# Kernel tuning notes

Hardware: AMD Instinct MI355X
Metric: run time of the kernel (lower is better)

## Reference

```python
import jax, jax.numpy as jnp
import numpy as np

D = 32      # bond_dim
N = 784     # 28*28 physical sites
HALF = 392  # single_rank = rank // 2
L = 10      # labels
B = 128     # batch


def setup_inputs() -> dict:
    key = jax.random.key(0)
    k0, k1, k2, k3, k4, k5 = jax.random.split(key, 6)
    # per-site 2-component input features; components sum to 1 so the
    # 392-step transfer-matrix product stays numerically stable in fp32
    u = jax.random.uniform(k0, (B, N), dtype=jnp.float32)
    x = jnp.stack([u, 1.0 - u], axis=-1)  # (B, 784, 2)

    eye = jnp.eye(D, dtype=jnp.float32)[None, :, None, :]  # (1, D, 1, D)
    a0 = jax.random.normal(k1, (D, 2), dtype=jnp.float32) / np.float32(np.sqrt(D))
    cores_left = eye + 0.01 * jax.random.normal(k2, (HALF - 1, D, 2, D), dtype=jnp.float32)
    core_mid = 0.05 * jax.random.normal(k3, (D, L, D), dtype=jnp.float32)
    cores_right = eye + 0.01 * jax.random.normal(k4, (HALF - 1, D, 2, D), dtype=jnp.float32)
    a_end = jax.random.normal(k5, (D, 2), dtype=jnp.float32) / np.float32(np.sqrt(D))
    return {"x": x, "a0": a0, "cores_left": cores_left, "core_mid": core_mid,
            "cores_right": cores_right, "a_end": a_end}


def reference(x, a0, cores_left, core_mid, cores_right, a_end):
    # ---- left half: nodes 0..391 contracted with inputs 0..391 ----
    v0 = jnp.einsum('dp,bp->bd', a0, x[:, 0])                       # (B, D)
    # input-contracted transfer matrices for nodes 1..391
    Ml = jnp.einsum('nlpr,bnp->nblr', cores_left, x[:, 1:HALF])      # (391, B, D, D)

    def step_left(c, M):
        return jnp.einsum('bl,blr->br', c, M), None

    left, _ = jax.lax.scan(step_left, v0, Ml)                        # (B, D)

    # ---- right half: nodes 393..784 contracted with inputs 392..783 ----
    r0 = jnp.einsum('dp,bp->bd', a_end, x[:, N - 1])                 # (B, D)
    Mr = jnp.einsum('nlpr,bnp->nblr', cores_right, x[:, HALF:N - 1])  # (391, B, D, D)

    def step_right(c, M):
        return jnp.einsum('blr,br->bl', M, c), None

    right, _ = jax.lax.scan(step_right, r0, Mr, reverse=True)        # (B, D)

    # ---- middle label node: original does einsum('a,aba,a->b') (diagonal!) ----
    mid_diag = jnp.einsum('aba->ab', core_mid)                       # (D, L)
    return jnp.einsum('ba,ba,ac->bc', left, right, mid_diag)         # (B, 10)
```

## Files before the change

kernel.cpp:

```cpp
#include <hip/hip_runtime.h>

#define NSTEP 391
#define NB 128
#define NGRP 16

typedef __attribute__((ext_vector_type(8))) short s8v;
typedef __attribute__((ext_vector_type(16))) float f32x16;

typedef const __attribute__((address_space(1))) void* gas_ptr;
typedef __attribute__((address_space(3))) void* las_ptr;

union I4S8 { int4 i; s8v v; };
union W4S8 { int w[4]; s8v v; };

#define WAITVM(N) do { asm volatile("s_waitcnt vmcnt(" #N ")" ::: "memory"); \
                       __builtin_amdgcn_sched_barrier(0); } while (0)
#define LGKM0     do { asm volatile("s_waitcnt lgkmcnt(0)" ::: "memory");   \
                       __builtin_amdgcn_sched_barrier(0); } while (0)
#define SBAR      do { __builtin_amdgcn_s_barrier();                        \
                       __builtin_amdgcn_sched_barrier(0); } while (0)

__device__ __forceinline__ int pack_hi(float a, float b) {
    return (__float_as_int(b) & 0xffff0000) | ((unsigned)__float_as_int(a) >> 16);
}
__device__ __forceinline__ float trunc_bf(float a) {
    return __int_as_float(__float_as_int(a) & 0xffff0000);
}
__device__ __forceinline__ int cvtpk(float a, float b) {
    int r;
    asm("v_cvt_pk_bf16_f32 %0, %1, %2" : "=v"(r) : "v"(a), "v"(b));
    return r;
}

__global__ __launch_bounds__(256) void prep(
    const float* __restrict__ coresL, const float* __restrict__ coresR,
    int* __restrict__ aprep) {
    const int bid = blockIdx.x;
    const int side = bid >= NSTEP;
    const int t = bid - side * NSTEP;
    const float* st = (side ? coresR : coresL) + t * 2048;
    int* out = aprep + (size_t)(side * NSTEP + t) * 2048;
    for (int o = threadIdx.x; o < 2048; o += 256) {
        const int f = o >> 8, lane = (o >> 2) & 63, w = o & 3;
        const int part = f >> 2, p = (f >> 1) & 1, j = f & 1;
        const int h = lane >> 5, c = lane & 31;
        const int k0 = j * 16 + h * 8 + w * 2;
        float e0, e1;
        if (!side) { e0 = st[c * 64 + p * 32 + k0];  e1 = st[c * 64 + p * 32 + k0 + 1]; }
        else       { e0 = st[k0 * 64 + p * 32 + c];  e1 = st[(k0 + 1) * 64 + p * 32 + c]; }
        out[o] = (part == 0) ? pack_hi(e0, e1)
                             : pack_hi(e0 - trunc_bf(e0), e1 - trunc_bf(e1));
    }
}

__device__ __forceinline__ void bpack(const float* d, bool h0, W4S8& b1h, W4S8& b2h,
                                      W4S8& b1l, W4S8& b2l) {
#if __has_builtin(__builtin_amdgcn_permlane32_swap)
    int hw[8], lw[8];
    #pragma unroll
    for (int q = 0; q < 8; ++q) {
        float e = d[2 * q], o = d[2 * q + 1];
        hw[q] = __builtin_amdgcn_perm(__float_as_uint(o), __float_as_uint(e), 0x07060302u);
        lw[q] = cvtpk(e - trunc_bf(e), o - trunc_bf(o));
    }
    {
        auto r0 = __builtin_amdgcn_permlane32_swap(hw[0], hw[2], false, false);
        b1h.w[0] = r0[0]; b1h.w[2] = r0[1];
        auto r1 = __builtin_amdgcn_permlane32_swap(hw[1], hw[3], false, false);
        b1h.w[1] = r1[0]; b1h.w[3] = r1[1];
        auto r2 = __builtin_amdgcn_permlane32_swap(hw[4], hw[6], false, false);
        b2h.w[0] = r2[0]; b2h.w[2] = r2[1];
        auto r3 = __builtin_amdgcn_permlane32_swap(hw[5], hw[7], false, false);
        b2h.w[1] = r3[0]; b2h.w[3] = r3[1];
        auto r4 = __builtin_amdgcn_permlane32_swap(lw[0], lw[2], false, false);
        b1l.w[0] = r4[0]; b1l.w[2] = r4[1];
        auto r5 = __builtin_amdgcn_permlane32_swap(lw[1], lw[3], false, false);
        b1l.w[1] = r5[0]; b1l.w[3] = r5[1];
        auto r6 = __builtin_amdgcn_permlane32_swap(lw[4], lw[6], false, false);
        b2l.w[0] = r6[0]; b2l.w[2] = r6[1];
        auto r7 = __builtin_amdgcn_permlane32_swap(lw[5], lw[7], false, false);
        b2l.w[1] = r7[0]; b2l.w[3] = r7[1];
    }
    (void)h0;
#else
    float sx[16];
    #pragma unroll
    for (int r = 0; r < 16; ++r) sx[r] = __shfl_xor(d[r], 32);
    float B1[8], B2[8];
    #pragma unroll
    for (int m = 0; m < 4; ++m) {
        B1[m]     = h0 ? d[m]      : sx[4 + m];
        B1[4 + m] = h0 ? sx[m]     : d[4 + m];
        B2[m]     = h0 ? d[8 + m]  : sx[12 + m];
        B2[4 + m] = h0 ? sx[8 + m] : d[12 + m];
    }
    #pragma unroll
    for (int ww = 0; ww < 4; ++ww) {
        b1h.w[ww] = pack_hi(B1[2 * ww], B1[2 * ww + 1]);
        b2h.w[ww] = pack_hi(B2[2 * ww], B2[2 * ww + 1]);
        b1l.w[ww] = cvtpk(B1[2 * ww] - trunc_bf(B1[2 * ww]),
                          B1[2 * ww + 1] - trunc_bf(B1[2 * ww + 1]));
        b2l.w[ww] = cvtpk(B2[2 * ww] - trunc_bf(B2[2 * ww]),
                          B2[2 * ww + 1] - trunc_bf(B2[2 * ww + 1]));
    }
#endif
}

__device__ __forceinline__ void mstep(float* d, const I4S8* fr,
                                      const W4S8& b1h, const W4S8& b2h,
                                      const W4S8& b1l, const W4S8& b2l, float2 xv) {
    f32x16 acc0 = {}; f32x16 acc1 = {};
    acc0 = __builtin_amdgcn_mfma_f32_32x32x16_bf16(fr[0].v, b1h.v, acc0, 0, 0, 0);
    acc1 = __builtin_amdgcn_mfma_f32_32x32x16_bf16(fr[2].v, b1h.v, acc1, 0, 0, 0);
    acc0 = __builtin_amdgcn_mfma_f32_32x32x16_bf16(fr[1].v, b2h.v, acc0, 0, 0, 0);
    acc1 = __builtin_amdgcn_mfma_f32_32x32x16_bf16(fr[3].v, b2h.v, acc1, 0, 0, 0);
    acc0 = __builtin_amdgcn_mfma_f32_32x32x16_bf16(fr[0].v, b1l.v, acc0, 0, 0, 0);
    acc1 = __builtin_amdgcn_mfma_f32_32x32x16_bf16(fr[2].v, b1l.v, acc1, 0, 0, 0);
    acc0 = __builtin_amdgcn_mfma_f32_32x32x16_bf16(fr[1].v, b2l.v, acc0, 0, 0, 0);
    acc1 = __builtin_amdgcn_mfma_f32_32x32x16_bf16(fr[3].v, b2l.v, acc1, 0, 0, 0);
    acc0 = __builtin_amdgcn_mfma_f32_32x32x16_bf16(fr[4].v, b1h.v, acc0, 0, 0, 0);
    acc1 = __builtin_amdgcn_mfma_f32_32x32x16_bf16(fr[6].v, b1h.v, acc1, 0, 0, 0);
    acc0 = __builtin_amdgcn_mfma_f32_32x32x16_bf16(fr[5].v, b2h.v, acc0, 0, 0, 0);
    acc1 = __builtin_amdgcn_mfma_f32_32x32x16_bf16(fr[7].v, b2h.v, acc1, 0, 0, 0);
    #pragma unroll
    for (int r = 0; r < 16; ++r) d[r] = fmaf(xv.y, acc1[r], xv.x * acc0[r]);
}

__device__ __forceinline__ void issue_part(const int* tb, int* slot, int lane, int wv) {
    const int f0 = wv * 2;
    __builtin_amdgcn_global_load_lds((gas_ptr)(tb + f0 * 256 + lane * 4),
                                     (las_ptr)(slot + f0 * 256), 16, 0, 0);
    __builtin_amdgcn_global_load_lds((gas_ptr)(tb + (f0 + 1) * 256 + lane * 4),
                                     (las_ptr)(slot + (f0 + 1) * 256), 16, 0, 0);
}

__global__ __launch_bounds__(256, 4) void stage1(
    const float* __restrict__ x, const int* __restrict__ aprep,
    float* __restrict__ qws) {
    __shared__ int ring[2][2048];
    __shared__ float2 xls[4][28];
    const int wv = threadIdx.x >> 6;
    const int lane = threadIdx.x & 63;
    const int dsp = blockIdx.x;
    const int xcd = dsp & 7;
    const int s = dsp >> 3;
    const int stream = xcd + 8 * (s & 3);
    const int inb = s >> 2;
    const int side = stream >> 4;
    const int g = stream & 15;
    const int b = inb * 4 + wv;
    const int a = g * 24 + (g < 7 ? g : 7);
    const int len = 24 + (g < 7 ? 1 : 0);
    const int h = lane >> 5, col = lane & 31;
    const bool h0 = (h == 0);

    const float2* xb2 = (const float2*)x + b * 784;
    if (lane < len) {
        int t = side ? (392 + a + lane) : (a + len - lane);
        xls[wv][lane] = xb2[t];
    }

    float d0[16];
    #pragma unroll
    for (int r = 0; r < 16; ++r)
        d0[r] = (((r & 3) + 8 * (r >> 2) + 4 * h) == col) ? 1.0f : 0.0f;

    const int* tbase = aprep + (size_t)side * NSTEP * 2048;
    auto taddr = [&](int j) {
        int t = side ? (a + j) : (a + len - 1 - j);
        t = t < 0 ? 0 : (t > 390 ? 390 : t);
        return tbase + (size_t)t * 2048;
    };

    issue_part(taddr(0), ring[0], lane, wv);
    issue_part(taddr(1), ring[1], lane, wv);

    for (int j = 0; j < len; ++j) {
        int* slot = ring[j & 1];
        W4S8 b1h, b2h, b1l, b2l;
        bpack(d0, h0, b1h, b2h, b1l, b2l);
        WAITVM(2);
        SBAR;
        I4S8 fr[8];
        #pragma unroll
        for (int f = 0; f < 8; ++f)
            fr[f].i = *(const int4*)(slot + f * 256 + lane * 4);
        mstep(d0, fr, b1h, b2h, b1l, b2l, xls[wv][j]);
        LGKM0;
        SBAR;
        issue_part(taddr(j + 2), slot, lane, wv);
    }
    WAITVM(0);

    float4* q0 = (float4*)(qws + (size_t)(side * 2048 + b * 16 + g) * 1024 + lane * 16);
    q0[0] = make_float4(d0[0], d0[1], d0[2], d0[3]);
    q0[1] = make_float4(d0[4], d0[5], d0[6], d0[7]);
    q0[2] = make_float4(d0[8], d0[9], d0[10], d0[11]);
    q0[3] = make_float4(d0[12], d0[13], d0[14], d0[15]);
}

__global__ __launch_bounds__(64) void stage2(
    const float* __restrict__ x, const float* __restrict__ a0,
    const float* __restrict__ aend, const float* __restrict__ qws,
    float* __restrict__ lw, float* __restrict__ rw) {
    const int b = blockIdx.x >> 1, side = blockIdx.x & 1;
    const int lane = threadIdx.x;
    const int j = lane >> 5, c = lane & 31;
    const float2* xb = (const float2*)x + b * 784;
    float v;
    if (side == 0) { float2 x0 = xb[0];   v = fmaf(a0[c * 2], x0.x, a0[c * 2 + 1] * x0.y); }
    else           { float2 xe = xb[783]; v = fmaf(aend[c * 2], xe.x, aend[c * 2 + 1] * xe.y); }
    for (int i = 0; i < NGRP; ++i) {
        const int g = side ? (NGRP - 1 - i) : i;
        const int task = side * 2048 + b * 16 + g;
        const float4* qp = (const float4*)(qws + (size_t)task * 1024 + (j * 32 + c) * 16);
        float q[16];
        #pragma unroll
        for (int u = 0; u < 4; ++u) {
            float4 t4 = qp[u];
            q[4 * u] = t4.x; q[4 * u + 1] = t4.y; q[4 * u + 2] = t4.z; q[4 * u + 3] = t4.w;
        }
        float s0 = 0.f, s1 = 0.f, s2 = 0.f, s3 = 0.f;
        #pragma unroll
        for (int r = 0; r < 16; r += 4) {
            s0 = fmaf(__shfl(v, 0 + 8 * (r >> 2) + 4 * j, 64), q[r + 0], s0);
            s1 = fmaf(__shfl(v, 1 + 8 * (r >> 2) + 4 * j, 64), q[r + 1], s1);
            s2 = fmaf(__shfl(v, 2 + 8 * (r >> 2) + 4 * j, 64), q[r + 2], s2);
            s3 = fmaf(__shfl(v, 3 + 8 * (r >> 2) + 4 * j, 64), q[r + 3], s3);
        }
        float s = (s0 + s1) + (s2 + s3);
        s += __shfl_xor(s, 32);
        v = s;
    }
    if (lane < 32) { (side ? rw : lw)[b * 32 + c] = v; }
}

__global__ __launch_bounds__(64) void mps_final(
    const float* __restrict__ lw, const float* __restrict__ rw,
    const float* __restrict__ mid,
    float* __restrict__ out) {
    const int b = blockIdx.x;
    const int a = threadIdx.x & 31;
    float pa = lw[b * 32 + a] * rw[b * 32 + a];
    #pragma unroll
    for (int c = 0; c < 10; ++c) {
        float s = pa * mid[a * 320 + c * 32 + a];
        s += __shfl_xor(s, 16, 32);
        s += __shfl_xor(s, 8, 32);
        s += __shfl_xor(s, 4, 32);
        s += __shfl_xor(s, 2, 32);
        s += __shfl_xor(s, 1, 32);
        if (threadIdx.x == 0) out[b * 10 + c] = s;
    }
}

extern "C" void kernel_launch(void* const* d_in, const int* in_sizes, int n_in,
                              void* d_out, int out_size, void* d_ws, size_t ws_size,
                              hipStream_t stream) {
    const float* x      = (const float*)d_in[0];
    const float* a0     = (const float*)d_in[1];
    const float* coresL = (const float*)d_in[2];
    const float* mid    = (const float*)d_in[3];
    const float* coresR = (const float*)d_in[4];
    const float* aend   = (const float*)d_in[5];

    int*   aprep = (int*)d_ws;
    float* qws   = (float*)d_ws + 2 * NSTEP * 2048;
    float* lw    = qws + 4096 * 1024;
    float* rw    = lw + NB * 32;
    float* out   = (float*)d_out;

    prep<<<dim3(2 * NSTEP), dim3(256), 0, stream>>>(coresL, coresR, aprep);
    stage1<<<dim3(1024), dim3(256), 0, stream>>>(x, aprep, qws);
    stage2<<<dim3(2 * NB), dim3(64), 0, stream>>>(x, a0, aend, qws, lw, rw);
    mps_final<<<dim3(NB), dim3(64), 0, stream>>>(lw, rw, mid, out);
}
```

Baseline: 67.26 us.

## Split chain into 32 segments, fuse stage2 with final, prefetch partials via LDS

Makes the segment count a template parameter and uses 32 segments per side when the workspace allows, doubling stage1 blocks and occupancy while shortening each serial chain. Stage2 now runs both sides in one block, prefetches the segment partial matrices into LDS with a double-buffered async load, and folds the final label contraction in, which removes one launch. In stage1 the next tile load is now issued before the MFMA step. The cost is a longer serial combine in stage2 (32 steps instead of 16) and more workspace traffic.

```diff
diff --git a/kernel.cpp b/kernel.cpp
--- a/kernel.cpp
+++ b/kernel.cpp
@@ -2,7 +2,6 @@
 
 #define NSTEP 391
 #define NB 128
-#define NGRP 16
 
 typedef __attribute__((ext_vector_type(8))) short s8v;
 typedef __attribute__((ext_vector_type(16))) float f32x16;
@@ -134,23 +133,26 @@
                                      (las_ptr)(slot + (f0 + 1) * 256), 16, 0, 0);
 }
 
-__global__ __launch_bounds__(256, 4) void stage1(
+template <int NG>
+__global__ __launch_bounds__(256, (NG == 32 ? 8 : 4)) void stage1(
     const float* __restrict__ x, const int* __restrict__ aprep,
     float* __restrict__ qws) {
     __shared__ int ring[2][2048];
     __shared__ float2 xls[4][28];
     const int wv = threadIdx.x >> 6;
     const int lane = threadIdx.x & 63;
+    constexpr int SPX = NG / 4;
     const int dsp = blockIdx.x;
     const int xcd = dsp & 7;
     const int s = dsp >> 3;
-    const int stream = xcd + 8 * (s & 3);
-    const int inb = s >> 2;
-    const int side = stream >> 4;
-    const int g = stream & 15;
+    const int stream = xcd + 8 * (s & (SPX - 1));
+    const int inb = s / SPX;
+    const int side = stream >= NG;
+    const int g = stream & (NG - 1);
     const int b = inb * 4 + wv;
-    const int a = g * 24 + (g < 7 ? g : 7);
-    const int len = 24 + (g < 7 ? 1 : 0);
+    constexpr int qq = NSTEP / NG, rr = NSTEP % NG;
+    const int a = g * qq + (g < rr ? g : rr);
+    const int len = qq + (g < rr ? 1 : 0);
     const int h = lane >> 5, col = lane & 31;
     const bool h0 = (h == 0);
 
@@ -168,7 +170,7 @@
     const int* tbase = aprep + (size_t)side * NSTEP * 2048;
     auto taddr = [&](int j) {
         int t = side ? (a + j) : (a + len - 1 - j);
-        t = t < 0 ? 0 : (t > 390 ? 390 : t);
+        t = t < 0 ? 0 : (t > NSTEP - 1 ? NSTEP - 1 : t);
         return tbase + (size_t)t * 2048;
     };
 
@@ -185,72 +187,95 @@
         #pragma unroll
         for (int f = 0; f < 8; ++f)
             fr[f].i = *(const int4*)(slot + f * 256 + lane * 4);
-        mstep(d0, fr, b1h, b2h, b1l, b2l, xls[wv][j]);
         LGKM0;
         SBAR;
         issue_part(taddr(j + 2), slot, lane, wv);
+        mstep(d0, fr, b1h, b2h, b1l, b2l, xls[wv][j]);
     }
     WAITVM(0);
 
-    float4* q0 = (float4*)(qws + (size_t)(side * 2048 + b * 16 + g) * 1024 + lane * 16);
+    float4* q0 = (float4*)(qws + ((size_t)(side * NB + b) * NG + g) * 1024 + lane * 16);
     q0[0] = make_float4(d0[0], d0[1], d0[2], d0[3]);
     q0[1] = make_float4(d0[4], d0[5], d0[6], d0[7]);
     q0[2] = make_float4(d0[8], d0[9], d0[10], d0[11]);
     q0[3] = make_float4(d0[12], d0[13], d0[14], d0[15]);
 }
 
-__global__ __launch_bounds__(64) void stage2(
+template <int NG>
+__global__ __launch_bounds__(64) void stage2f(
     const float* __restrict__ x, const float* __restrict__ a0,
     const float* __restrict__ aend, const float* __restrict__ qws,
-    float* __restrict__ lw, float* __restrict__ rw) {
-    const int b = blockIdx.x >> 1, side = blockIdx.x & 1;
+    const float* __restrict__ mid, float* __restrict__ out) {
+    __shared__ float ring[2][2048];
+    const int b = blockIdx.x;
     const int lane = threadIdx.x;
-    const int j = lane >> 5, c = lane & 31;
+    const int c = lane & 31;
+    const int j = lane >> 5;
     const float2* xb = (const float2*)x + b * 784;
-    float v;
-    if (side == 0) { float2 x0 = xb[0];   v = fmaf(a0[c * 2], x0.x, a0[c * 2 + 1] * x0.y); }
-    else           { float2 xe = xb[783]; v = fmaf(aend[c * 2], xe.x, aend[c * 2 + 1] * xe.y); }
-    for (int i = 0; i < NGRP; ++i) {
-        const int g = side ? (NGRP - 1 - i) : i;
-        const int task = side * 2048 + b * 16 + g;
-        const float4* qp = (const float4*)(qws + (size_t)task * 1024 + (j * 32 + c) * 16);
-        float q[16];
+    float2 x0 = xb[0], xe = xb[783];
+    float v0 = fmaf(a0[c * 2], x0.x, a0[c * 2 + 1] * x0.y);
+    float v1 = fmaf(aend[c * 2], xe.x, aend[c * 2 + 1] * xe.y);
+
+    auto issue = [&](int i, float* slot) {
+        int ic = i < NG - 1 ? i : NG - 1;
+        const float* t0 = qws + ((size_t)b * NG + ic) * 1024;
+        const float* t1 = qws + ((size_t)(NB + b) * NG + (NG - 1 - ic)) * 1024;
         #pragma unroll
         for (int u = 0; u < 4; ++u) {
-            float4 t4 = qp[u];
-            q[4 * u] = t4.x; q[4 * u + 1] = t4.y; q[4 * u + 2] = t4.z; q[4 * u + 3] = t4.w;
+            __builtin_amdgcn_global_load_lds((gas_ptr)(t0 + u * 256 + lane * 4),
+                                             (las_ptr)(slot + u * 256), 16, 0, 0);
+            __builtin_amdgcn_global_load_lds((gas_ptr)(t1 + u * 256 + lane * 4),
+                                             (las_ptr)(slot + 1024 + u * 256), 16, 0, 0);
         }
+    };
+    issue(0, ring[0]);
+    issue(1, ring[1]);
+
+    for (int i = 0; i < NG; ++i) {
+        float* slot = ring[i & 1];
+        WAITVM(8);
+        float q0[16], q1[16];
+        #pragma unroll
+        for (int u = 0; u < 4; ++u) {
+            float4 t4 = *(const float4*)(slot + lane * 16 + u * 4);
+            q0[4 * u] = t4.x; q0[4 * u + 1] = t4.y; q0[4 * u + 2] = t4.z; q0[4 * u + 3] = t4.w;
+            float4 t5 = *(const float4*)(slot + 1024 + lane * 16 + u * 4);
+            q1[4 * u] = t5.x; q1[4 * u + 1] = t5.y; q1[4 * u + 2] = t5.z; q1[4 * u + 3] = t5.w;
+        }
+        LGKM0;
+        issue(i + 2, slot);
         float s0 = 0.f, s1 = 0.f, s2 = 0.f, s3 = 0.f;
+        float u0 = 0.f, u1 = 0.f, u2 = 0.f, u3 = 0.f;
         #pragma unroll
         for (int r = 0; r < 16; r += 4) {
-            s0 = fmaf(__shfl(v, 0 + 8 * (r >> 2) + 4 * j, 64), q[r + 0], s0);
-            s1 = fmaf(__shfl(v, 1 + 8 * (r >> 2) + 4 * j, 64), q[r + 1], s1);
-            s2 = fmaf(__shfl(v, 2 + 8 * (r >> 2) + 4 * j, 64), q[r + 2], s2);
-            s3 = fmaf(__shfl(v, 3 + 8 * (r >> 2) + 4 * j, 64), q[r + 3], s3);
+            const int base = 8 * (r >> 2) + 4 * j;
+            s0 = fmaf(__shfl(v0, base + 0, 64), q0[r + 0], s0);
+            u0 = fmaf(__shfl(v1, base + 0, 64), q1[r + 0], u0);
+            s1 = fmaf(__shfl(v0, base + 1, 64), q0[r + 1], s1);
+            u1 = fmaf(__shfl(v1, base + 1, 64), q1[r + 1], u1);
+            s2 = fmaf(__shfl(v0, base + 2, 64), q0[r + 2], s2);
+            u2 = fmaf(__shfl(v1, base + 2, 64), q1[r + 2], u2);
+            s3 = fmaf(__shfl(v0, base + 3, 64), q0[r + 3], s3);
+            u3 = fmaf(__shfl(v1, base + 3, 64), q1[r + 3], u3);
         }
-        float s = (s0 + s1) + (s2 + s3);
-        s += __shfl_xor(s, 32);
-        v = s;
-    }
-    if (lane < 32) { (side ? rw : lw)[b * 32 + c] = v; }
-}
-
-__global__ __launch_bounds__(64) void mps_final(
-    const float* __restrict__ lw, const float* __restrict__ rw,
-    const float* __restrict__ mid,
-    float* __restrict__ out) {
-    const int b = blockIdx.x;
-    const int a = threadIdx.x & 31;
-    float pa = lw[b * 32 + a] * rw[b * 32 + a];
-    #pragma unroll
-    for (int c = 0; c < 10; ++c) {
-        float s = pa * mid[a * 320 + c * 32 + a];
+        float sv = (s0 + s1) + (s2 + s3);
+        float uv = (u0 + u1) + (u2 + u3);
+        sv += __shfl_xor(sv, 32);
+        uv += __shfl_xor(uv, 32);
+        v0 = sv; v1 = uv;
+    }
+    WAITVM(0);
+
+    float pa = v0 * v1;
+    #pragma unroll
+    for (int cc = 0; cc < 10; ++cc) {
+        float s = pa * mid[c * 320 + cc * 32 + c];
         s += __shfl_xor(s, 16, 32);
         s += __shfl_xor(s, 8, 32);
         s += __shfl_xor(s, 4, 32);
         s += __shfl_xor(s, 2, 32);
         s += __shfl_xor(s, 1, 32);
-        if (threadIdx.x == 0) out[b * 10 + c] = s;
+        if (lane == 0) out[b * 10 + cc] = s;
     }
 }
 
@@ -266,12 +291,17 @@
 
     int*   aprep = (int*)d_ws;
     float* qws   = (float*)d_ws + 2 * NSTEP * 2048;
-    float* lw    = qws + 4096 * 1024;
-    float* rw    = lw + NB * 32;
     float* out   = (float*)d_out;
 
+    const size_t need32 = (size_t)(2 * NSTEP * 2048) * 4
+                        + (size_t)2 * NB * 32 * 1024 * 4;
+
     prep<<<dim3(2 * NSTEP), dim3(256), 0, stream>>>(coresL, coresR, aprep);
-    stage1<<<dim3(1024), dim3(256), 0, stream>>>(x, aprep, qws);
-    stage2<<<dim3(2 * NB), dim3(64), 0, stream>>>(x, a0, aend, qws, lw, rw);
-    mps_final<<<dim3(NB), dim3(64), 0, stream>>>(lw, rw, mid, out);
-}
+    if (ws_size >= need32) {
+        stage1<32><<<dim3(2048), dim3(256), 0, stream>>>(x, aprep, qws);
+        stage2f<32><<<dim3(NB), dim3(64), 0, stream>>>(x, a0, aend, qws, mid, out);
+    } else {
+        stage1<16><<<dim3(1024), dim3(256), 0, stream>>>(x, aprep, qws);
+        stage2f<16><<<dim3(NB), dim3(64), 0, stream>>>(x, a0, aend, qws, mid, out);
+    }
+}
```

Measured after the change: 143.4 us. 2.13x slower.
